# Kernel tuning notes

Hardware: AMD Instinct MI355X
Metric: run time of the kernel (lower is better)

## Reference

```python
import jax, jax.numpy as jnp
from jax import lax
import numpy as np

TAO, M, C_IN, D_MODEL = 3, 5, 7, 512
KERNELS = D_MODEL // C_IN            # 73
EXTRA = D_MODEL - C_IN * KERNELS     # 1


def setup_inputs() -> dict:
    key = jax.random.key(0)
    k1, k2, k3, k4, k5 = jax.random.split(key, 5)
    B, S = 32, 4096
    x = jax.random.normal(k1, (B, S, C_IN), dtype=jnp.float32)
    fan_in = (M + 1) * 3
    scale = jnp.float32(np.sqrt(2.0 / fan_in))  # kaiming-ish
    group_w = jax.random.normal(k2, (C_IN * KERNELS, M + 1, 3), dtype=jnp.float32) * scale
    group_b = jax.random.normal(k3, (C_IN * KERNELS,), dtype=jnp.float32) * 0.01
    left_w = jax.random.normal(k4, (EXTRA, M + 1, 3), dtype=jnp.float32) * scale
    left_b = jax.random.normal(k5, (EXTRA,), dtype=jnp.float32) * 0.01
    return {"x": x, "group_w": group_w, "group_b": group_b,
            "left_w": left_w, "left_b": left_b}


def _circular_conv1d(x_ncl, w_oik, groups):
    # kernel_size=3, padding=1, padding_mode='circular' -> wrap-pad then VALID conv
    xp = jnp.pad(x_ncl, ((0, 0), (0, 0), (1, 1)), mode="wrap")
    return lax.conv_general_dilated(
        xp, w_oik, window_strides=(1,), padding="VALID",
        dimension_numbers=("NCH", "OIH", "NCH"),
        feature_group_count=groups)


def reference(x, group_w, group_b, left_w, left_b):
    B, S, C = x.shape
    warm = M * TAO
    # vectorized delay-embedding gather: faithful vec at time t is
    # [ts[t - i*tao, c] for c in channels for i in 0..m]  (channel-major)
    times = jnp.arange(warm, S)                              # [T']
    lags = times[:, None] - TAO * jnp.arange(M + 1)[None, :]  # [T', m+1]
    g = x[:, lags, :]                                        # [B, T', m+1, C]
    g = jnp.transpose(g, (0, 1, 3, 2)).reshape(B, S - warm, C * (M + 1))
    # pad warmup region with zeros at the front of the time axis
    g = jnp.pad(g, ((0, 0), (warm, 0), (0, 0)))              # [B, S, C*(m+1)]
    e = jnp.transpose(g, (0, 2, 1))                          # [B, C*(m+1), S]
    conv = _circular_conv1d(e, group_w, groups=C_IN) + group_b[None, :, None]
    # leftout conv on the last channel's delay block
    last = e.reshape(B, C_IN, M + 1, S)[:, -1]               # [B, m+1, S]
    extra = _circular_conv1d(last, left_w, groups=1) + left_b[None, :, None]
    out = jnp.concatenate([conv, extra], axis=1)             # [B, d_model, S]
    return jnp.transpose(out, (0, 2, 1))                     # [B, S, d_model]
```

## Files before the change

### kernel.cpp

```cpp
#include <hip/hip_runtime.h>

#define S_LEN 4096
#define B_SZ 32
#define C_IN 7
#define D_MODEL 512
#define TL 64
#define CH 8
#define NCH (TL / CH)

__global__ __launch_bounds__(512)
void fir_main(const float* __restrict__ x,
              const float* __restrict__ gw,
              const float* __restrict__ gb,
              const float* __restrict__ lw,
              const float* __restrict__ lb,
              float* __restrict__ out)
{
    __shared__ float ws[512 * 18];
    __shared__ float wb[512];
    __shared__ float xs[7][88];

    const int tid = threadIdx.x;
    const int n   = blockIdx.x;
    const int l0  = blockIdx.y * TL;

    for (int i = tid; i < 512 * 18; i += 512)
        ws[i] = (i < 511 * 18) ? gw[i] : lw[i - 511 * 18];
    wb[tid] = (tid < 511) ? gb[tid] : lb[0];

    for (int i = tid; i < 81 * 7; i += 512) {
        int t = i / 7, c = i - t * 7;
        int tg = l0 - 16 + t;
        tg = tg < 0 ? 0 : (tg > S_LEN - 1 ? S_LEN - 1 : tg);
        xs[c][t] = x[((size_t)n * S_LEN + tg) * C_IN + c];
    }
    __syncthreads();

    const int o = tid;
    const int c = (o < 511) ? (o / 73) : 6;
    float wf[18];
#pragma unroll
    for (int j = 0; j < 6; ++j)
#pragma unroll
        for (int k = 0; k < 3; ++k)
            wf[15 + k - 3 * j] = ws[o * 18 + j * 3 + k];
    const float bias = wb[o];

    float* op = out + ((size_t)n * S_LEN + l0) * D_MODEL + o;

#pragma unroll
    for (int ci = 0; ci < NCH; ++ci) {
        float xv[28];
        const float* xb = &xs[c][ci * CH];
#pragma unroll
        for (int q = 0; q < 7; ++q) {
            float4 v = *(const float4*)(xb + q * 4);
            xv[q * 4 + 0] = v.x; xv[q * 4 + 1] = v.y;
            xv[q * 4 + 2] = v.z; xv[q * 4 + 3] = v.w;
        }
#pragma unroll
        for (int u = 0; u < CH; ++u) {
            float acc = bias;
#pragma unroll
            for (int d = 0; d < 18; ++d)
                acc = fmaf(wf[d], xv[u + d], acc);
            op[(size_t)(ci * CH + u) * D_MODEL] = acc;
        }
    }
}

__global__ __launch_bounds__(512)
void fir_fixup(const float* __restrict__ x,
               const float* __restrict__ gw,
               const float* __restrict__ gb,
               const float* __restrict__ lw,
               const float* __restrict__ lb,
               float* __restrict__ out)
{
    const int o  = threadIdx.x;
    const int n  = blockIdx.x;
    const int li = blockIdx.y;
    const int l  = (li < 16) ? li : (S_LEN - 1);

    const int c = (o < 511) ? (o / 73) : 6;
    const float* wsrc = (o < 511) ? (gw + o * 18) : lw;
    float acc = (o < 511) ? gb[o] : lb[0];

    const float* xc = x + (size_t)n * S_LEN * C_IN + c;
#pragma unroll
    for (int j = 0; j < 6; ++j) {
#pragma unroll
        for (int k = 0; k < 3; ++k) {
            int t = l - 1 + k;
            if (t < 0) t += S_LEN;
            if (t >= S_LEN) t -= S_LEN;
            if (t >= 15)
                acc = fmaf(wsrc[j * 3 + k], xc[(size_t)(t - 3 * j) * C_IN], acc);
        }
    }
    out[((size_t)n * S_LEN + l) * D_MODEL + o] = acc;
}

extern "C" void kernel_launch(void* const* d_in, const int* in_sizes, int n_in,
                              void* d_out, int out_size, void* d_ws, size_t ws_size,
                              hipStream_t stream)
{
    const float* x  = (const float*)d_in[0];
    const float* gw = (const float*)d_in[1];
    const float* gb = (const float*)d_in[2];
    const float* lw = (const float*)d_in[3];
    const float* lb = (const float*)d_in[4];
    float* out = (float*)d_out;

    dim3 grid_main(B_SZ, S_LEN / TL);
    fir_main<<<grid_main, 512, 0, stream>>>(x, gw, gb, lw, lb, out);

    dim3 grid_fix(B_SZ, 17);
    fir_fixup<<<grid_fix, 512, 0, stream>>>(x, gw, gb, lw, lb, out);
}
```

Baseline: 284.5 us.

## Fuse boundary fixup into main FIR kernel and double time tile

Removes the separate fixup kernel launch. The first and last time-tile blocks of the main kernel now recompute the warmup rows and the circular-wrap row in place after the main pass. The time tile grows from 64 to 128, which halves how often each block reloads the 36 KB weight table into shared memory. In exchange the grid has fewer blocks, and the boundary blocks do serialized extra work with uncoalesced global loads of x.

```diff
diff --git a/kernel.cpp b/kernel.cpp
--- a/kernel.cpp
+++ b/kernel.cpp
@@ -4,31 +4,32 @@
 #define B_SZ 32
 #define C_IN 7
 #define D_MODEL 512
-#define TL 64
+#define TL 128
 #define CH 8
 #define NCH (TL / CH)
+#define WIN (TL + 17)
+#define XROW 148
 
 __global__ __launch_bounds__(512)
-void fir_main(const float* __restrict__ x,
-              const float* __restrict__ gw,
-              const float* __restrict__ gb,
-              const float* __restrict__ lw,
-              const float* __restrict__ lb,
-              float* __restrict__ out)
+void fir_fused(const float* __restrict__ x,
+               const float* __restrict__ gw,
+               const float* __restrict__ gb,
+               const float* __restrict__ lw,
+               const float* __restrict__ lb,
+               float* __restrict__ out)
 {
     __shared__ float ws[512 * 18];
-    __shared__ float wb[512];
-    __shared__ float xs[7][88];
+    __shared__ float xs[7][XROW];
 
     const int tid = threadIdx.x;
     const int n   = blockIdx.x;
-    const int l0  = blockIdx.y * TL;
+    const int by  = blockIdx.y;
+    const int l0  = by * TL;
 
     for (int i = tid; i < 512 * 18; i += 512)
         ws[i] = (i < 511 * 18) ? gw[i] : lw[i - 511 * 18];
-    wb[tid] = (tid < 511) ? gb[tid] : lb[0];
 
-    for (int i = tid; i < 81 * 7; i += 512) {
+    for (int i = tid; i < WIN * C_IN; i += 512) {
         int t = i / 7, c = i - t * 7;
         int tg = l0 - 16 + t;
         tg = tg < 0 ? 0 : (tg > S_LEN - 1 ? S_LEN - 1 : tg);
@@ -44,7 +45,7 @@
 #pragma unroll
         for (int k = 0; k < 3; ++k)
             wf[15 + k - 3 * j] = ws[o * 18 + j * 3 + k];
-    const float bias = wb[o];
+    const float bias = (o < 511) ? gb[o] : lb[0];
 
     float* op = out + ((size_t)n * S_LEN + l0) * D_MODEL + o;
 
@@ -67,38 +68,40 @@
             op[(size_t)(ci * CH + u) * D_MODEL] = acc;
         }
     }
-}
 
-__global__ __launch_bounds__(512)
-void fir_fixup(const float* __restrict__ x,
-               const float* __restrict__ gw,
-               const float* __restrict__ gb,
-               const float* __restrict__ lw,
-               const float* __restrict__ lb,
-               float* __restrict__ out)
-{
-    const int o  = threadIdx.x;
-    const int n  = blockIdx.x;
-    const int li = blockIdx.y;
-    const int l  = (li < 16) ? li : (S_LEN - 1);
-
-    const int c = (o < 511) ? (o / 73) : 6;
-    const float* wsrc = (o < 511) ? (gw + o * 18) : lw;
-    float acc = (o < 511) ? gb[o] : lb[0];
-
-    const float* xc = x + (size_t)n * S_LEN * C_IN + c;
+    if (by == 0) {
+#pragma unroll 1
+        for (int l = 0; l < 16; ++l) {
+            float acc = bias;
 #pragma unroll
-    for (int j = 0; j < 6; ++j) {
+            for (int j = 0; j < 6; ++j)
 #pragma unroll
-        for (int k = 0; k < 3; ++k) {
-            int t = l - 1 + k;
-            if (t < 0) t += S_LEN;
-            if (t >= S_LEN) t -= S_LEN;
-            if (t >= 15)
-                acc = fmaf(wsrc[j * 3 + k], xc[(size_t)(t - 3 * j) * C_IN], acc);
+                for (int k = 0; k < 3; ++k) {
+                    int t = l - 1 + k;
+                    if (t < 0) t += S_LEN;
+                    if (t >= 15)
+                        acc = fmaf(ws[o * 18 + j * 3 + k],
+                                   x[((size_t)n * S_LEN + (t - 3 * j)) * C_IN + c],
+                                   acc);
+                }
+            out[((size_t)n * S_LEN + l) * D_MODEL + o] = acc;
         }
+    } else if (by == (S_LEN / TL) - 1) {
+        const int l = S_LEN - 1;
+        float acc = bias;
+#pragma unroll
+        for (int j = 0; j < 6; ++j)
+#pragma unroll
+            for (int k = 0; k < 3; ++k) {
+                int t = l - 1 + k;
+                if (t >= S_LEN) t -= S_LEN;
+                if (t >= 15)
+                    acc = fmaf(ws[o * 18 + j * 3 + k],
+                               x[((size_t)n * S_LEN + (t - 3 * j)) * C_IN + c],
+                               acc);
+            }
+        out[((size_t)n * S_LEN + l) * D_MODEL + o] = acc;
     }
-    out[((size_t)n * S_LEN + l) * D_MODEL + o] = acc;
 }
 
 extern "C" void kernel_launch(void* const* d_in, const int* in_sizes, int n_in,
@@ -112,9 +115,6 @@
     const float* lb = (const float*)d_in[4];
     float* out = (float*)d_out;
 
-    dim3 grid_main(B_SZ, S_LEN / TL);
-    fir_main<<<grid_main, 512, 0, stream>>>(x, gw, gb, lw, lb, out);
-
-    dim3 grid_fix(B_SZ, 17);
-    fir_fixup<<<grid_fix, 512, 0, stream>>>(x, gw, gb, lw, lb, out);
+    dim3 grid(B_SZ, S_LEN / TL);
+    fir_fused<<<grid, 512, 0, stream>>>(x, gw, gb, lw, lb, out);
 }
```

After: 278.4 us. -2.2%, faster.
